# Performance work log

Measured on AMD Instinct MI355X. Metric: run time of the kernel, lower is better.

Reference implementation:

```python
import jax, jax.numpy as jnp
import numpy as np

D_MODEL = 512
N_HEADS = 8
B, S = 2, 2048


def setup_inputs() -> dict:
    key = jax.random.key(0)
    ks = jax.random.split(key, 7)
    scale = 1.0 / np.sqrt(D_MODEL)
    return {
        "q": jax.random.normal(ks[0], (B, S, D_MODEL), jnp.float32),
        "k": jax.random.normal(ks[1], (B, S, D_MODEL), jnp.float32),
        "v": jax.random.normal(ks[2], (B, S, D_MODEL), jnp.float32),
        "Wq_w": jax.random.normal(ks[3], (D_MODEL, D_MODEL), jnp.float32) * scale,
        "Wq_b": jnp.zeros((D_MODEL,), jnp.float32),
        "Wc_w": jax.random.normal(ks[4], (D_MODEL, D_MODEL), jnp.float32) * scale,
        "Wc_b": jnp.zeros((D_MODEL,), jnp.float32),
    }


def _split(x, n_heads):
    b, s, d = x.shape
    return x.reshape(b, s, n_heads, d // n_heads).transpose(0, 2, 1, 3)  # [b,h,s,dh]


def reference(q, k, v, Wq_w, Wq_b, Wc_w, Wc_b):
    # NOTE: original code (faithfully) projects q, k, v all with W_q.
    qp = q @ Wq_w.T + Wq_b
    kp = k @ Wq_w.T + Wq_b
    vp = v @ Wq_w.T + Wq_b
    qh = _split(qp, N_HEADS)  # [b,h,s,dh]
    kh = _split(kp, N_HEADS)
    vh = _split(vp, N_HEADS)
    d_tensor = qh.shape[-1]
    scores = jnp.einsum("bhqd,bhkd->bhqk", qh, kh) / jnp.sqrt(jnp.float32(d_tensor))
    att = jax.nn.softmax(scores, axis=-1)
    out = jnp.einsum("bhqk,bhkd->bhqd", att, vh)
    b, h, s, dh = out.shape
    out = out.transpose(0, 2, 1, 3).reshape(b, s, h * dh)
    return out @ Wc_w.T + Wc_b
```

## Files before the change

### kernel.cpp

```cpp
#include <hip/hip_runtime.h>
#include <hip/hip_bf16.h>
#include <stdint.h>


typedef __bf16 bf16;
typedef __bf16 bvec8 __attribute__((ext_vector_type(8)));
typedef __bf16 bvec4 __attribute__((ext_vector_type(4)));
typedef float  fvec4 __attribute__((ext_vector_type(4)));
typedef float  fvec16 __attribute__((ext_vector_type(16)));
typedef int    ivec4 __attribute__((ext_vector_type(4)));

#define MFMA16(a, b, c) __builtin_amdgcn_mfma_f32_16x16x32_bf16(a, b, c, 0, 0, 0)
#define MFMA32(a, b, c) __builtin_amdgcn_mfma_f32_32x32x16_bf16(a, b, c, 0, 0, 0)

__device__ __forceinline__ void async16(const void* g, void* l) {
  __builtin_amdgcn_global_load_lds(
      (__attribute__((address_space(1))) void*)(g),
      (__attribute__((address_space(3))) void*)(l), 16, 0, 0);
}

__global__ void cvt_all(const float* __restrict__ q, const float* __restrict__ k,
                        const float* __restrict__ v, const float* __restrict__ Wq,
                        const float* __restrict__ Wc, bf16* __restrict__ qkvb,
                        bf16* __restrict__ Wq16, bf16* __restrict__ Wc16) {
  const int t = blockIdx.x * 256 + threadIdx.x;
  const float* src;
  bf16* dst;
  size_t i;
  if (t < 786432) {
    const int which = t >> 18;
    i = (size_t)(t & 262143);
    src = (which == 0) ? q : (which == 1) ? k : v;
    dst = qkvb + ((size_t)which << 21);
  } else if (t < 819200) {
    src = Wq; dst = Wq16; i = (size_t)(t - 786432);
  } else {
    src = Wc; dst = Wc16; i = (size_t)(t - 819200);
  }
  fvec4 a = *(const fvec4*)(src + i * 8);
  fvec4 b = *(const fvec4*)(src + i * 8 + 4);
  bvec8 o;
#pragma unroll
  for (int j = 0; j < 4; ++j) { o[j] = (bf16)a[j]; o[j + 4] = (bf16)b[j]; }
  *(bvec8*)(dst + i * 8) = o;
}

__launch_bounds__(256, 3)
__global__ void proj_gemm(const bf16* __restrict__ X, const bf16* __restrict__ W,
                          const float* __restrict__ bias, bf16* __restrict__ Y,
                          bf16* __restrict__ Yt) {
  __shared__ __attribute__((aligned(16))) char As[2][64 * 128];
  __shared__ __attribute__((aligned(16))) char Bs[2][128 * 128];

  const int tid = threadIdx.x;
  const int w = tid >> 6, l = tid & 63;
  const int wr = w >> 1, wc = w & 1;
  const int l15 = l & 15, lg = l >> 4;
  const int bm0 = blockIdx.x * 64;
  const int bn0 = blockIdx.y * 128;

  fvec4 acc[2][4] = {};

  auto stageA = [&](int buf, int k0) {
#pragma unroll
    for (int j = 0; j < 2; ++j) {
      int c = j * 256 + tid;
      int row = c >> 3, g = (c & 7) ^ (row & 7);
      async16(X + (size_t)(bm0 + row) * 512 + k0 + g * 8, &As[buf][c * 16]);
    }
  };
  auto stageB = [&](int buf, int k0) {
#pragma unroll
    for (int j = 0; j < 4; ++j) {
      int c = j * 256 + tid;
      int row = c >> 3, g = (c & 7) ^ (row & 7);
      async16(W + (size_t)(bn0 + row) * 512 + k0 + g * 8, &Bs[buf][c * 16]);
    }
  };

  stageA(0, 0);
  stageB(0, 0);
  __syncthreads();

  for (int t = 0; t < 8; ++t) {
    const int buf = t & 1;
    if (t < 7) { stageA(buf ^ 1, (t + 1) * 64); stageB(buf ^ 1, (t + 1) * 64); }
#pragma unroll
    for (int kk = 0; kk < 2; ++kk) {
      bvec8 af[2], bfr[4];
      const int g = kk * 4 + lg;
#pragma unroll
      for (int m = 0; m < 2; ++m) {
        int r = wr * 32 + m * 16 + l15;
        af[m] = *(const bvec8*)&As[buf][r * 128 + ((g ^ (r & 7)) << 4)];
      }
#pragma unroll
      for (int n = 0; n < 4; ++n) {
        int r = wc * 64 + n * 16 + l15;
        bfr[n] = *(const bvec8*)&Bs[buf][r * 128 + ((g ^ (r & 7)) << 4)];
      }
#pragma unroll
      for (int m = 0; m < 2; ++m)
#pragma unroll
        for (int n = 0; n < 4; ++n) acc[m][n] = MFMA16(af[m], bfr[n], acc[m][n]);
    }
    __syncthreads();
  }

  const bool trans = (bm0 >= 8192);
  const float scl = (bm0 < 4096) ? 0.18033688011112042f : 1.0f;
#pragma unroll
  for (int n = 0; n < 4; ++n) {
    const int col = bn0 + wc * 64 + n * 16 + l15;
    const float bv = bias[col];
#pragma unroll
    for (int m = 0; m < 2; ++m) {
      const int row0 = bm0 + wr * 32 + m * 16 + lg * 4;
      if (!trans) {
#pragma unroll
        for (int r = 0; r < 4; ++r)
          Y[(size_t)(row0 + r) * 512 + col] = (bf16)((acc[m][n][r] + bv) * scl);
      } else {
        const int m0 = row0 - 8192;
        const int b = m0 >> 11, s = m0 & 2047;
        bvec4 v4;
#pragma unroll
        for (int r = 0; r < 4; ++r) v4[r] = (bf16)(acc[m][n][r] + bv);
        *(bvec4*)&Yt[(size_t)(b * 512 + col) * 2048 + s] = v4;
      }
    }
  }
}

__launch_bounds__(256, 2)
__global__ void attn_kernel(const bf16* __restrict__ qp, const bf16* __restrict__ kp,
                            const bf16* __restrict__ vt, bf16* __restrict__ po,
                            float* __restrict__ pl) {
  __shared__ __attribute__((aligned(16))) char Ks[4][64 * 128];
  __shared__ __attribute__((aligned(16))) char Vs[4][64 * 128];

  const int tid = threadIdx.x;
  const int w = tid >> 6, l = tid & 63;
  const int l31 = l & 31, hi = l >> 5;
  const int bh = blockIdx.y, b = bh >> 3, h = bh & 7;
  const int half = blockIdx.z;
  const int kvbase = half * 1024;
  const int qw0 = blockIdx.x * 128 + w * 32;

  const bf16* kbase = kp + (size_t)(b * 2048) * 512 + h * 64;
  const bf16* vbase = vt + (size_t)(b * 512 + h * 64) * 2048;

  bvec8 qf[4];
  {
    const bf16* qrow = qp + (size_t)(b * 2048 + qw0 + l31) * 512 + h * 64 + hi * 8;
#pragma unroll
    for (int ks = 0; ks < 4; ++ks) qf[ks] = *(const bvec8*)(qrow + ks * 16);
  }
  bvec8 ones;
#pragma unroll
  for (int e = 0; e < 8; ++e) ones[e] = (bf16)1.0f;

  auto stage = [&](int buf, int kv0) {
#pragma unroll
    for (int j = 0; j < 2; ++j) {
      int c = j * 256 + tid;
      int row = c >> 3, g = (c & 7) ^ (row & 7);
      async16(kbase + (size_t)(kv0 + row) * 512 + g * 8, &Ks[buf][c * 16]);
    }
#pragma unroll
    for (int j = 0; j < 2; ++j) {
      int c = j * 256 + tid;
      int row = c >> 3, g = (c & 7) ^ (row & 7);
      async16(vbase + (size_t)row * 2048 + kv0 + g * 8, &Vs[buf][c * 16]);
    }
  };

  fvec16 oacc[2] = {};
  fvec16 lacc = {};
  fvec16 sac[2][2];

  auto QK = [&](int sb, int buf) {
    sac[sb][0] = fvec16{};
    sac[sb][1] = fvec16{};
    __builtin_amdgcn_s_setprio(1);
#pragma unroll
    for (int ks = 0; ks < 4; ++ks) {
      const int chunk = ks * 2 + hi;
#pragma unroll
      for (int kvb = 0; kvb < 2; ++kvb) {
        const int r = kvb * 32 + l31;
        bvec8 kf = *(const bvec8*)&Ks[buf][r * 128 + ((chunk ^ (r & 7)) << 4)];
        sac[sb][kvb] = MFMA32(kf, qf[ks], sac[sb][kvb]);
      }
    }
    __builtin_amdgcn_s_setprio(0);
  };

  stage(0, kvbase);
  stage(1, kvbase + 64);
  stage(2, kvbase + 128);
  asm volatile("s_waitcnt vmcnt(8)" ::: "memory");
  __builtin_amdgcn_sched_barrier(0);
  __builtin_amdgcn_s_barrier();
  QK(0, 0);

#pragma unroll
  for (int t = 0; t < 16; ++t) {
    const int sb = t & 1;
    const int buf = t & 3;

    if (t < 15) {
      if (t < 14) asm volatile("s_waitcnt vmcnt(4)" ::: "memory");
      else        asm volatile("s_waitcnt vmcnt(0)" ::: "memory");
      __builtin_amdgcn_sched_barrier(0);
      __builtin_amdgcn_s_barrier();
      if (t < 13) stage((t + 3) & 3, kvbase + (t + 3) * 64);
      QK(sb ^ 1, (t + 1) & 3);
    }

    ivec4 pw[4];
#pragma unroll
    for (int f = 0; f < 2; ++f) {
      float p[16];
#pragma unroll
      for (int r2 = 0; r2 < 16; ++r2) p[r2] = exp2f(sac[sb][f][r2]);
      int wv[4][2];
#pragma unroll
      for (int m = 0; m < 4; ++m)
#pragma unroll
        for (int i = 0; i < 2; ++i)
          asm("v_cvt_pk_bf16_f32 %0, %1, %2"
              : "=v"(wv[m][i]) : "v"(p[4 * m + 2 * i]), "v"(p[4 * m + 2 * i + 1]));
#pragma unroll
      for (int i = 0; i < 2; ++i) {
        int a0 = wv[0][i], c0 = wv[1][i];
        asm volatile("v_permlane32_swap_b32 %0, %1" : "+v"(a0), "+v"(c0));
        pw[2 * f][i] = a0; pw[2 * f][2 + i] = c0;
        int a1 = wv[2][i], c1 = wv[3][i];
        asm volatile("v_permlane32_swap_b32 %0, %1" : "+v"(a1), "+v"(c1));
        pw[2 * f + 1][i] = a1; pw[2 * f + 1][2 + i] = c1;
      }
    }

    __builtin_amdgcn_s_setprio(1);
#pragma unroll
    for (int ks = 0; ks < 4; ++ks) {
      const bvec8 pb = __builtin_bit_cast(bvec8, pw[ks]);
      const int chunk = ks * 2 + hi;
#pragma unroll
      for (int dhb = 0; dhb < 2; ++dhb) {
        const int r = dhb * 32 + l31;
        bvec8 vf = *(const bvec8*)&Vs[buf][r * 128 + ((chunk ^ (r & 7)) << 4)];
        oacc[dhb] = MFMA32(pb, vf, oacc[dhb]);
      }
      lacc = MFMA32(pb, ones, lacc);
    }
    __builtin_amdgcn_s_setprio(0);
  }

  bf16* pob = po + (size_t)half * 2097152;
#pragma unroll
  for (int dhb = 0; dhb < 2; ++dhb)
#pragma unroll
    for (int r2 = 0; r2 < 16; ++r2) {
      const int q = qw0 + (r2 & 3) + 8 * (r2 >> 2) + 4 * hi;
      pob[(size_t)(b * 2048 + q) * 512 + h * 64 + dhb * 32 + l31] =
          (bf16)oacc[dhb][r2];
    }
  if (l31 == 0) {
#pragma unroll
    for (int r2 = 0; r2 < 16; ++r2) {
      const int q = qw0 + (r2 & 3) + 8 * (r2 >> 2) + 4 * hi;
      pl[half * 32768 + (b * 2048 + q) * 8 + h] = lacc[r2];
    }
  }
}

__global__ void combine_kernel(const bf16* __restrict__ po, const float* __restrict__ pl,
                               bf16* __restrict__ att) {
  const int t = blockIdx.x * 256 + threadIdx.x;
  const int row = t >> 6;
  const int c8 = (t & 63) << 3;
  const int h = c8 >> 6;
  const float inv = 1.0f / (pl[row * 8 + h] + pl[32768 + row * 8 + h]);
  bvec8 a0 = *(const bvec8*)(po + (size_t)row * 512 + c8);
  bvec8 a1 = *(const bvec8*)(po + 2097152 + (size_t)row * 512 + c8);
  bvec8 o;
#pragma unroll
  for (int j = 0; j < 8; ++j)
    o[j] = (bf16)(((float)a0[j] + (float)a1[j]) * inv);
  *(bvec8*)(att + (size_t)row * 512 + c8) = o;
}

__launch_bounds__(256, 3)
__global__ void out_gemm(const bf16* __restrict__ X, const bf16* __restrict__ W,
                         const float* __restrict__ bias, float* __restrict__ Y) {
  __shared__ __attribute__((aligned(16))) char As[2][64 * 128];
  __shared__ __attribute__((aligned(16))) char Bs[2][128 * 128];

  const int tid = threadIdx.x;
  const int w = tid >> 6, l = tid & 63;
  const int wr = w >> 1, wc = w & 1;
  const int l15 = l & 15, lg = l >> 4;
  const int bm0 = blockIdx.x * 64;
  const int bn0 = blockIdx.y * 128;

  fvec4 acc[2][4] = {};

  auto stageA = [&](int buf, int k0) {
#pragma unroll
    for (int j = 0; j < 2; ++j) {
      int c = j * 256 + tid;
      int row = c >> 3, g = (c & 7) ^ (row & 7);
      async16(X + (size_t)(bm0 + row) * 512 + k0 + g * 8, &As[buf][c * 16]);
    }
  };
  auto stageB = [&](int buf, int k0) {
#pragma unroll
    for (int j = 0; j < 4; ++j) {
      int c = j * 256 + tid;
      int row = c >> 3, g = (c & 7) ^ (row & 7);
      async16(W + (size_t)(bn0 + row) * 512 + k0 + g * 8, &Bs[buf][c * 16]);
    }
  };

  stageA(0, 0);
  stageB(0, 0);
  __syncthreads();

  for (int t = 0; t < 8; ++t) {
    const int buf = t & 1;
    if (t < 7) { stageA(buf ^ 1, (t + 1) * 64); stageB(buf ^ 1, (t + 1) * 64); }
#pragma unroll
    for (int kk = 0; kk < 2; ++kk) {
      bvec8 af[2], bfr[4];
      const int g = kk * 4 + lg;
#pragma unroll
      for (int m = 0; m < 2; ++m) {
        int r = wr * 32 + m * 16 + l15;
        af[m] = *(const bvec8*)&As[buf][r * 128 + ((g ^ (r & 7)) << 4)];
      }
#pragma unroll
      for (int n = 0; n < 4; ++n) {
        int r = wc * 64 + n * 16 + l15;
        bfr[n] = *(const bvec8*)&Bs[buf][r * 128 + ((g ^ (r & 7)) << 4)];
      }
#pragma unroll
      for (int m = 0; m < 2; ++m)
#pragma unroll
        for (int n = 0; n < 4; ++n) acc[m][n] = MFMA16(af[m], bfr[n], acc[m][n]);
    }
    __syncthreads();
  }

#pragma unroll
  for (int n = 0; n < 4; ++n) {
    const int col = bn0 + wc * 64 + n * 16 + l15;
    const float bv = bias[col];
#pragma unroll
    for (int m = 0; m < 2; ++m) {
      const int row0 = bm0 + wr * 32 + m * 16 + lg * 4;
#pragma unroll
      for (int r = 0; r < 4; ++r)
        Y[(size_t)(row0 + r) * 512 + col] = acc[m][n][r] + bv;
    }
  }
}

extern "C" void kernel_launch(void* const* d_in, const int* in_sizes, int n_in,
                              void* d_out, int out_size, void* d_ws, size_t ws_size,
                              hipStream_t stream) {
  const float* q   = (const float*)d_in[0];
  const float* k   = (const float*)d_in[1];
  const float* v   = (const float*)d_in[2];
  const float* Wq  = (const float*)d_in[3];
  const float* Wqb = (const float*)d_in[4];
  const float* Wc  = (const float*)d_in[5];
  const float* Wcb = (const float*)d_in[6];
  float* out = (float*)d_out;

  char* ws = (char*)d_ws;
  const size_t MB = 1u << 20;
  bf16* qkvb = (bf16*)(ws);
  bf16* po   = (bf16*)(ws);
  bf16* att  = (bf16*)(ws + 8 * MB);
  bf16* Wq16 = (bf16*)(ws + 12 * MB);
  bf16* Wc16 = (bf16*)(ws + 12 * MB + 512 * 1024);
  bf16* qkp  = (bf16*)(ws + 13 * MB);
  bf16* vt   = (bf16*)(ws + 21 * MB);
  float* pl  = (float*)(ws + 33 * MB);

  dim3 bb(256);
  hipLaunchKernelGGL(cvt_all, dim3(3328), bb, 0, stream, q, k, v, Wq, Wc,
                     qkvb, Wq16, Wc16);
  hipLaunchKernelGGL(proj_gemm, dim3(192, 4), bb, 0, stream,
                     qkvb, Wq16, Wqb, qkp, vt);
  hipLaunchKernelGGL(attn_kernel, dim3(16, 16, 2), bb, 0, stream,
                     qkp, qkp + 2097152, vt, po, pl);
  hipLaunchKernelGGL(combine_kernel, dim3(1024), bb, 0, stream, po, pl, att);
  hipLaunchKernelGGL(out_gemm, dim3(64, 4), bb, 0, stream,
                     att, Wc16, Wcb, out);
}
```

Before: 68.43 us.

## Fuse split-KV combine into output GEMM A-tile load and reorder softmax exp

Removes the separate combine kernel. The output GEMM now loads both partial attention outputs and their row sums into registers, normalises them and writes the bf16 A tile into shared memory, overlapping this with the MFMA work on the current buffer. This saves one launch and the round trip through the att buffer. In exchange the A tile goes through registers instead of async global-to-LDS copies, and each of the four column blocks repeats the combine arithmetic. Separately, the exp/convert/permute of the current score tile is moved ahead of the barrier and next QK issue in the attention loop, which may overlap differently with the wait.

```diff
diff --git a/kernel.cpp b/kernel.cpp
--- a/kernel.cpp
+++ b/kernel.cpp
@@ -209,6 +209,30 @@
     const int sb = t & 1;
     const int buf = t & 3;
 
+    ivec4 pw[4];
+#pragma unroll
+    for (int f = 0; f < 2; ++f) {
+      float p[16];
+#pragma unroll
+      for (int r2 = 0; r2 < 16; ++r2) p[r2] = exp2f(sac[sb][f][r2]);
+      int wv[4][2];
+#pragma unroll
+      for (int m = 0; m < 4; ++m)
+#pragma unroll
+        for (int i = 0; i < 2; ++i)
+          asm("v_cvt_pk_bf16_f32 %0, %1, %2"
+              : "=v"(wv[m][i]) : "v"(p[4 * m + 2 * i]), "v"(p[4 * m + 2 * i + 1]));
+#pragma unroll
+      for (int i = 0; i < 2; ++i) {
+        int a0 = wv[0][i], c0 = wv[1][i];
+        asm volatile("v_permlane32_swap_b32 %0, %1" : "+v"(a0), "+v"(c0));
+        pw[2 * f][i] = a0; pw[2 * f][2 + i] = c0;
+        int a1 = wv[2][i], c1 = wv[3][i];
+        asm volatile("v_permlane32_swap_b32 %0, %1" : "+v"(a1), "+v"(c1));
+        pw[2 * f + 1][i] = a1; pw[2 * f + 1][2 + i] = c1;
+      }
+    }
+
     if (t < 15) {
       if (t < 14) asm volatile("s_waitcnt vmcnt(4)" ::: "memory");
       else        asm volatile("s_waitcnt vmcnt(0)" ::: "memory");
@@ -218,30 +242,6 @@
       QK(sb ^ 1, (t + 1) & 3);
     }
 
-    ivec4 pw[4];
-#pragma unroll
-    for (int f = 0; f < 2; ++f) {
-      float p[16];
-#pragma unroll
-      for (int r2 = 0; r2 < 16; ++r2) p[r2] = exp2f(sac[sb][f][r2]);
-      int wv[4][2];
-#pragma unroll
-      for (int m = 0; m < 4; ++m)
-#pragma unroll
-        for (int i = 0; i < 2; ++i)
-          asm("v_cvt_pk_bf16_f32 %0, %1, %2"
-              : "=v"(wv[m][i]) : "v"(p[4 * m + 2 * i]), "v"(p[4 * m + 2 * i + 1]));
-#pragma unroll
-      for (int i = 0; i < 2; ++i) {
-        int a0 = wv[0][i], c0 = wv[1][i];
-        asm volatile("v_permlane32_swap_b32 %0, %1" : "+v"(a0), "+v"(c0));
-        pw[2 * f][i] = a0; pw[2 * f][2 + i] = c0;
-        int a1 = wv[2][i], c1 = wv[3][i];
-        asm volatile("v_permlane32_swap_b32 %0, %1" : "+v"(a1), "+v"(c1));
-        pw[2 * f + 1][i] = a1; pw[2 * f + 1][2 + i] = c1;
-      }
-    }
-
     __builtin_amdgcn_s_setprio(1);
 #pragma unroll
     for (int ks = 0; ks < 4; ++ks) {
@@ -276,25 +276,10 @@
   }
 }
 
-__global__ void combine_kernel(const bf16* __restrict__ po, const float* __restrict__ pl,
-                               bf16* __restrict__ att) {
-  const int t = blockIdx.x * 256 + threadIdx.x;
-  const int row = t >> 6;
-  const int c8 = (t & 63) << 3;
-  const int h = c8 >> 6;
-  const float inv = 1.0f / (pl[row * 8 + h] + pl[32768 + row * 8 + h]);
-  bvec8 a0 = *(const bvec8*)(po + (size_t)row * 512 + c8);
-  bvec8 a1 = *(const bvec8*)(po + 2097152 + (size_t)row * 512 + c8);
-  bvec8 o;
-#pragma unroll
-  for (int j = 0; j < 8; ++j)
-    o[j] = (bf16)(((float)a0[j] + (float)a1[j]) * inv);
-  *(bvec8*)(att + (size_t)row * 512 + c8) = o;
-}
-
 __launch_bounds__(256, 3)
-__global__ void out_gemm(const bf16* __restrict__ X, const bf16* __restrict__ W,
-                         const float* __restrict__ bias, float* __restrict__ Y) {
+__global__ void out_gemm(const bf16* __restrict__ po, const float* __restrict__ pl,
+                         const bf16* __restrict__ W, const float* __restrict__ bias,
+                         float* __restrict__ Y) {
   __shared__ __attribute__((aligned(16))) char As[2][64 * 128];
   __shared__ __attribute__((aligned(16))) char Bs[2][128 * 128];
 
@@ -306,13 +291,32 @@
   const int bn0 = blockIdx.y * 128;
 
   fvec4 acc[2][4] = {};
-
-  auto stageA = [&](int buf, int k0) {
+  bvec8 rp[2][2];
+  float rl[2][2];
+
+  auto loadA = [&](int k0) {
 #pragma unroll
     for (int j = 0; j < 2; ++j) {
       int c = j * 256 + tid;
       int row = c >> 3, g = (c & 7) ^ (row & 7);
-      async16(X + (size_t)(bm0 + row) * 512 + k0 + g * 8, &As[buf][c * 16]);
+      const size_t off = (size_t)(bm0 + row) * 512 + k0 + g * 8;
+      rp[j][0] = *(const bvec8*)(po + off);
+      rp[j][1] = *(const bvec8*)(po + 2097152 + off);
+      const int ridx = (bm0 + row) * 8 + ((k0 + g * 8) >> 6);
+      rl[j][0] = pl[ridx];
+      rl[j][1] = pl[32768 + ridx];
+    }
+  };
+  auto writeA = [&](int buf) {
+#pragma unroll
+    for (int j = 0; j < 2; ++j) {
+      int c = j * 256 + tid;
+      const float inv = 1.0f / (rl[j][0] + rl[j][1]);
+      bvec8 o;
+#pragma unroll
+      for (int e = 0; e < 8; ++e)
+        o[e] = (bf16)(((float)rp[j][0][e] + (float)rp[j][1][e]) * inv);
+      *(bvec8*)&As[buf][c * 16] = o;
     }
   };
   auto stageB = [&](int buf, int k0) {
@@ -324,13 +328,17 @@
     }
   };
 
-  stageA(0, 0);
+  loadA(0);
   stageB(0, 0);
+  writeA(0);
   __syncthreads();
 
   for (int t = 0; t < 8; ++t) {
     const int buf = t & 1;
-    if (t < 7) { stageA(buf ^ 1, (t + 1) * 64); stageB(buf ^ 1, (t + 1) * 64); }
+    if (t < 7) {
+      loadA((t + 1) * 64);
+      stageB(buf ^ 1, (t + 1) * 64);
+    }
 #pragma unroll
     for (int kk = 0; kk < 2; ++kk) {
       bvec8 af[2], bfr[4];
@@ -350,6 +358,7 @@
 #pragma unroll
         for (int n = 0; n < 4; ++n) acc[m][n] = MFMA16(af[m], bfr[n], acc[m][n]);
     }
+    if (t < 7) writeA(buf ^ 1);
     __syncthreads();
   }
 
@@ -383,7 +392,6 @@
   const size_t MB = 1u << 20;
   bf16* qkvb = (bf16*)(ws);
   bf16* po   = (bf16*)(ws);
-  bf16* att  = (bf16*)(ws + 8 * MB);
   bf16* Wq16 = (bf16*)(ws + 12 * MB);
   bf16* Wc16 = (bf16*)(ws + 12 * MB + 512 * 1024);
   bf16* qkp  = (bf16*)(ws + 13 * MB);
@@ -397,7 +405,6 @@
                      qkvb, Wq16, Wqb, qkp, vt);
   hipLaunchKernelGGL(attn_kernel, dim3(16, 16, 2), bb, 0, stream,
                      qkp, qkp + 2097152, vt, po, pl);
-  hipLaunchKernelGGL(combine_kernel, dim3(1024), bb, 0, stream, po, pl, att);
   hipLaunchKernelGGL(out_gemm, dim3(64, 4), bb, 0, stream,
-                     att, Wc16, Wcb, out);
-}
+                     po, pl, Wc16, Wcb, out);
+}
```

Result: no change. 68.37 us (-0.1%).
